# Performance work log

Hardware: AMD Instinct MI355X
Metric: run time of the kernel (lower is better)

The kernel has to match this reference:

```python
import jax, jax.numpy as jnp
import numpy as np

D_MODEL = 512
D_STATE = 64
HEADDIM = 64
EXPAND = 2
D_CONV = 4
D_INNER = EXPAND * D_MODEL            # 1024
NHEADS = D_INNER // HEADDIM           # 16
CONV_DIM = D_INNER + 2 * D_STATE      # 1152 (x, B, C share the depthwise conv)
D_IN_PROJ = 2 * D_INNER + 2 * D_STATE + NHEADS  # z, xBC, dt
C_IN = 512


def setup_inputs() -> dict:
    key = jax.random.key(0)
    ks = jax.random.split(key, 10)
    hs = jax.random.normal(ks[0], (1, C_IN, 16, 16, 16), jnp.float32)
    return {
        "hidden_states": hs,
        # 1x1 conv projections (weight stored as (out,in))
        "proj_in_w": jax.random.normal(ks[1], (D_MODEL, C_IN), jnp.float32) / np.float32(np.sqrt(C_IN)),
        "proj_in_b": jnp.zeros((D_MODEL,), jnp.float32),
        "proj_out_w": jax.random.normal(ks[2], (C_IN, D_MODEL), jnp.float32) * jnp.float32(0.02),
        "proj_out_b": jnp.zeros((C_IN,), jnp.float32),
        # Mamba2 core params
        "in_proj_w": jax.random.normal(ks[3], (D_IN_PROJ, D_MODEL), jnp.float32) / np.float32(np.sqrt(D_MODEL)),
        "conv_w": jax.random.normal(ks[4], (CONV_DIM, D_CONV), jnp.float32) / np.float32(np.sqrt(D_CONV)),
        "conv_b": jnp.zeros((CONV_DIM,), jnp.float32),
        "dt_bias": jnp.log(jnp.expm1(jax.random.uniform(ks[5], (NHEADS,), jnp.float32, 1e-3, 0.1))),
        "A_log": jnp.log(jax.random.uniform(ks[6], (NHEADS,), jnp.float32, 1.0, 16.0)),
        "D": jnp.ones((NHEADS,), jnp.float32),
        "norm_w": jnp.ones((D_INNER,), jnp.float32),
        "out_proj_w": jax.random.normal(ks[7], (D_MODEL, D_INNER), jnp.float32) / np.float32(np.sqrt(D_INNER)),
    }


def _mamba2(x, in_proj_w, conv_w, conv_b, dt_bias, A_log, Dp, norm_w, out_proj_w):
    # x: (N, T, d_model) with N = B*H*W (independent pixel sequences over time)
    N, T, _ = x.shape
    zxbcdt = jnp.einsum('ntd,ed->nte', x, in_proj_w)  # (N,T,D_IN_PROJ)
    z = zxbcdt[..., :D_INNER]
    xBC = zxbcdt[..., D_INNER:D_INNER + CONV_DIM]
    dt = zxbcdt[..., D_INNER + CONV_DIM:]             # (N,T,NHEADS)
    # causal depthwise conv along T (kernel D_CONV, left-padded), then SiLU
    pad = jnp.pad(xBC, ((0, 0), (D_CONV - 1, 0), (0, 0)))
    xc = sum(pad[:, k:k + T, :] * conv_w[:, k] for k in range(D_CONV))
    xBC = jax.nn.silu(xc + conv_b)
    xs = xBC[..., :D_INNER].reshape(N, T, NHEADS, HEADDIM)
    Bm = xBC[..., D_INNER:D_INNER + D_STATE]          # (N,T,D_STATE), ngroups=1
    Cm = xBC[..., D_INNER + D_STATE:]                 # (N,T,D_STATE)
    dt = jax.nn.softplus(dt + dt_bias)                # (N,T,NHEADS)
    A = -jnp.exp(A_log)                               # (NHEADS,)

    def step(h, inp):
        # h: (N, NHEADS, HEADDIM, D_STATE)
        dt_t, x_t, B_t, C_t = inp
        dA = jnp.exp(dt_t * A)                        # (N,NHEADS)
        h = h * dA[:, :, None, None] + (dt_t[:, :, None] * x_t)[..., None] * B_t[:, None, None, :]
        y_t = jnp.einsum('nhps,ns->nhp', h, C_t)      # (N,NHEADS,HEADDIM)
        return h, y_t

    h0 = jnp.zeros((N, NHEADS, HEADDIM, D_STATE), x.dtype)
    _, ys = jax.lax.scan(step, h0, (dt.swapaxes(0, 1), xs.swapaxes(0, 1), Bm.swapaxes(0, 1), Cm.swapaxes(0, 1)))
    y = ys.swapaxes(0, 1) + Dp[None, None, :, None] * xs   # skip term
    # gated RMSNorm: norm(y * silu(z)) * weight
    y = y.reshape(N, T, D_INNER) * jax.nn.silu(z)
    y = y * jax.lax.rsqrt(jnp.mean(y * y, axis=-1, keepdims=True) + 1e-5) * norm_w
    return jnp.einsum('ntd,od->nto', y, out_proj_w)


def reference(hidden_states, proj_in_w, proj_in_b, proj_out_w, proj_out_b,
              in_proj_w, conv_w, conv_b, dt_bias, A_log, D, norm_w, out_proj_w):
    B, C, T, H, W = hidden_states.shape
    # proj_in: 1x1 conv over channels == per-pixel matmul
    x = jnp.einsum('bcthw,dc->bthwd', hidden_states, proj_in_w) + proj_in_b
    # (B,T,H,W,D) -> (B*H*W, T, D): each pixel becomes a temporal sequence
    x = x.transpose(0, 2, 3, 1, 4).reshape(B * H * W, T, D_MODEL)
    y = _mamba2(x, in_proj_w, conv_w, conv_b, dt_bias, A_log, D, norm_w, out_proj_w)
    y = y.reshape(B, H, W, T, D_MODEL).transpose(0, 3, 1, 2, 4)  # (B,T,H,W,D)
    out = jnp.einsum('bthwd,cd->bcthw', y, proj_out_w) + proj_out_b[None, :, None, None, None]
    return (out,)
```

## Files before the change

kernel.cpp:

```cpp
#include <hip/hip_runtime.h>
#include <hip/hip_bf16.h>
#include <math.h>

#define TT       16
#define NSEQ     256
#define TOK      4096
#define DMODEL   512
#define DINNER   1024
#define DSTATE   64
#define NHEADS   16
#define HEADDIM  64
#define CONVDIM  1152
#define DINPROJ  2192
#define DTOFF    2176
#define ZLD      2176
#define NPAD_IP  2304

using bf16x8 = __attribute__((ext_vector_type(8))) short;
using f32x4  = __attribute__((ext_vector_type(4))) float;
typedef __hip_bfloat16 bf16;

__device__ __forceinline__ void gload_lds16(const void* g, void* l) {
    __builtin_amdgcn_global_load_lds(
        (const __attribute__((address_space(1))) unsigned int*)g,
        (__attribute__((address_space(3))) unsigned int*)l,
        16, 0, 0);
}

template<int NFRAG, bool OUTBF, bool DUAL, int BIAS, bool PARTSCALE>
__global__ __launch_bounds__(256) void mfma_gemm(
    const bf16* __restrict__ A, const bf16* __restrict__ B,
    const float* __restrict__ bias, const float* __restrict__ rs,
    float* __restrict__ Cf, bf16* __restrict__ Ch, float* __restrict__ C2,
    int Nreal, int K, int lda, int ldb, int ldc)
{
    constexpr int BN = NFRAG * 32;
    __shared__ short As[128 * 32];
    __shared__ short Bs[BN * 32];

    const int tid = threadIdx.x;
    const int wv = tid >> 6, ln = tid & 63;
    const int m0 = blockIdx.x * 128, n0 = blockIdx.y * BN;
    const int wr = wv >> 1, wc = wv & 1;
    const int lr = ln & 15, lk = (ln >> 4) * 8;

    f32x4 acc[4][NFRAG];
#pragma unroll
    for (int m = 0; m < 4; ++m)
#pragma unroll
        for (int n = 0; n < NFRAG; ++n) acc[m][n] = (f32x4){0.f, 0.f, 0.f, 0.f};

    for (int k0 = 0; k0 < K; k0 += 32) {
        __syncthreads();
#pragma unroll
        for (int r = 0; r < 2; ++r) {
            const int ofs = r * 4096 + tid * 16;
            const int row = ofs >> 6;
            const int ke  = (ofs & 63) >> 1;
            gload_lds16(A + (size_t)(m0 + row) * lda + k0 + ke, (char*)As + ofs);
        }
#pragma unroll
        for (int r = 0; r < NFRAG / 2; ++r) {
            const int ofs = r * 4096 + tid * 16;
            const int row = ofs >> 6;
            const int ke  = (ofs & 63) >> 1;
            gload_lds16(B + (size_t)(n0 + row) * ldb + k0 + ke, (char*)Bs + ofs);
        }
        __syncthreads();

        bf16x8 af[4], bfr[NFRAG];
#pragma unroll
        for (int m = 0; m < 4; ++m)
            af[m] = *(const bf16x8*)&As[(wr * 64 + m * 16 + lr) * 32 + lk];
#pragma unroll
        for (int n = 0; n < NFRAG; ++n)
            bfr[n] = *(const bf16x8*)&Bs[(wc * (BN / 2) + n * 16 + lr) * 32 + lk];
#pragma unroll
        for (int m = 0; m < 4; ++m)
#pragma unroll
            for (int n = 0; n < NFRAG; ++n)
                acc[m][n] = __builtin_amdgcn_mfma_f32_16x16x32_bf16(
                    af[m], bfr[n], acc[m][n], 0, 0, 0);
    }

    const int mBase = m0 + wr * 64, nBase = n0 + wc * (BN / 2);
#pragma unroll
    for (int m = 0; m < 4; ++m) {
#pragma unroll
        for (int j = 0; j < 4; ++j) {
            const int row = mBase + m * 16 + (ln >> 4) * 4 + j;
            float sc = 1.f, rb = 0.f;
            if (PARTSCALE) {
                const float4 pv = *(const float4*)(rs + (size_t)row * 4);
                sc = rsqrtf((pv.x + pv.y + pv.z + pv.w) * (1.f / 1024.f) + 1e-5f);
            }
            if (BIAS == 2) rb = bias[row];
#pragma unroll
            for (int n = 0; n < NFRAG; ++n) {
                const int col = nBase + n * 16 + lr;
                if (col < Nreal) {
                    float v = acc[m][n][j];
                    if (BIAS == 1) v += bias[col];
                    v += rb;
                    if (PARTSCALE) v *= sc;
                    if (OUTBF) {
                        Ch[(size_t)row * ldc + col] = __float2bfloat16(v);
                        if (DUAL) C2[(size_t)row * ldc + col] = v;
                    } else {
                        Cf[(size_t)row * ldc + col] = v;
                    }
                }
            }
        }
    }
}

#define SZ_PI  (512 * 512)
#define SZ_PO  (512 * 512)
#define SZ_OP  (512 * 1024)
#define SZ_IP  (DINPROJ * 512)
#define SZ_IPP (NPAD_IP * 512)
#define SZ_ALL (SZ_PI + SZ_PO + SZ_OP + SZ_IPP)
#define NB_WB  1024
#define NB_HT  2048

__global__ __launch_bounds__(256) void prep_all(
    const float* __restrict__ pi, const float* __restrict__ po,
    const float* __restrict__ op, const float* __restrict__ ip,
    const float* __restrict__ nw, const float* __restrict__ hs,
    bf16* __restrict__ wpi, bf16* __restrict__ wpo,
    bf16* __restrict__ wop, bf16* __restrict__ wip, bf16* __restrict__ hsT)
{
    __shared__ float smem[32 * 33];
    const int b = blockIdx.x, tid = threadIdx.x;

    if (b < NB_WB) {
        for (int idx = b * 256 + tid; idx < SZ_ALL; idx += NB_WB * 256) {
            if (idx < SZ_PI) {
                wpi[idx] = __float2bfloat16(pi[idx]);
            } else if (idx < SZ_PI + SZ_PO) {
                int j = idx - SZ_PI; wpo[j] = __float2bfloat16(po[j]);
            } else if (idx < SZ_PI + SZ_PO + SZ_OP) {
                int j = idx - SZ_PI - SZ_PO;
                wop[j] = __float2bfloat16(op[j] * nw[j & 1023]);
            } else {
                int j = idx - SZ_PI - SZ_PO - SZ_OP;
                wip[j] = (j < SZ_IP) ? __float2bfloat16(ip[j])
                                     : __float2bfloat16(0.f);
            }
        }
    } else {
        const int tb = b - NB_WB;
        const int v0 = (tb & 127) * 32, c0 = (tb >> 7) * 32;
        const int tx = tid & 31, ty = tid >> 5;
#pragma unroll
        for (int i = 0; i < 4; ++i)
            smem[(ty + 8 * i) * 33 + tx] =
                hs[(size_t)(c0 + ty + 8 * i) * TOK + v0 + tx];
        __syncthreads();
#pragma unroll
        for (int i = 0; i < 4; ++i)
            hsT[(size_t)(v0 + ty + 8 * i) * DMODEL + c0 + tx] =
                __float2bfloat16(smem[tx * 33 + ty + 8 * i]);
    }
}

__global__ __launch_bounds__(256) void dt_fix_kernel(
    const float* __restrict__ xv32, const float* __restrict__ in_proj_w,
    float* __restrict__ dtf)
{
    const int v = blockIdx.x;
    const int w = threadIdx.x >> 6, l = threadIdx.x & 63;
    const float4* xr = (const float4*)(xv32 + (size_t)v * DMODEL);
    const float4 x0 = xr[l * 2], x1 = xr[l * 2 + 1];
#pragma unroll
    for (int hh = 0; hh < 4; ++hh) {
        const int h = w * 4 + hh;
        const float4* wr = (const float4*)(in_proj_w + (size_t)(DTOFF + h) * DMODEL);
        const float4 w0 = wr[l * 2], w1 = wr[l * 2 + 1];
        float dot = x0.x * w0.x + x0.y * w0.y + x0.z * w0.z + x0.w * w0.w
                  + x1.x * w1.x + x1.y * w1.y + x1.z * w1.z + x1.w * w1.w;
#pragma unroll
        for (int off = 32; off >= 1; off >>= 1) dot += __shfl_xor(dot, off);
        if (l == 0) dtf[(size_t)v * 16 + h] = dot;
    }
}

__global__ __launch_bounds__(256) void ssd_kernel(
    const bf16* __restrict__ zb, const float* __restrict__ dtf,
    const float* __restrict__ conv_w, const float* __restrict__ conv_b,
    const float* __restrict__ dt_bias, const float* __restrict__ A_log,
    const float* __restrict__ Dp,
    bf16* __restrict__ gb, float* __restrict__ part)
{
    const int n = blockIdx.x, hq = blockIdx.y;
    const int tid = threadIdx.x;
    const int w = tid >> 6, p = tid & 63;
    const int h = hq * 4 + w;
    const int ch = hq * 256 + tid;

    __shared__ float Bsh[16][68];
    __shared__ float Csh[16][68];
    __shared__ float Gsh[16][16];
    __shared__ float Msh[4][256];
    __shared__ float red4[16][4];

    float ld[16];
#pragma unroll
    for (int t = 0; t < 16; ++t)
        ld[t] = __bfloat162float(zb[(size_t)(t * 256 + n) * ZLD + 1024 + ch]);

    const float cw0 = conv_w[ch * 4 + 0], cw1 = conv_w[ch * 4 + 1],
                cw2 = conv_w[ch * 4 + 2], cw3 = conv_w[ch * 4 + 3];
    const float cb = conv_b[ch];
    float xs[16];
#pragma unroll
    for (int t = 0; t < 16; ++t) {
        float a = fmaf(ld[t], cw3, cb);
        if (t >= 1) a = fmaf(ld[t - 1], cw2, a);
        if (t >= 2) a = fmaf(ld[t - 2], cw1, a);
        if (t >= 3) a = fmaf(ld[t - 3], cw0, a);
        xs[t] = a / (1.f + __expf(-a));
    }

    if (tid < 128) {
        const int cc = 1024 + tid;
        const float dw0 = conv_w[cc * 4 + 0], dw1 = conv_w[cc * 4 + 1],
                    dw2 = conv_w[cc * 4 + 2], dw3 = conv_w[cc * 4 + 3];
        const float db = conv_b[cc];
        float q0 = 0.f, q1 = 0.f, q2 = 0.f;
#pragma unroll
        for (int t = 0; t < 16; ++t) {
            const float cur =
                __bfloat162float(zb[(size_t)(t * 256 + n) * ZLD + 2048 + tid]);
            float a = fmaf(cur, dw3, db);
            a = fmaf(q2, dw2, a);
            a = fmaf(q1, dw1, a);
            a = fmaf(q0, dw0, a);
            const float val = a / (1.f + __expf(-a));
            if (tid < 64) Bsh[t][tid] = val; else Csh[t][tid - 64] = val;
            q0 = q1; q1 = q2; q2 = cur;
        }
    }

    const float a_h = -__expf(A_log[h]);
    float dtv_l = 0.f;
    if (p < 16) {
        const float raw = dtf[(size_t)(p * 256 + n) * 16 + h] + dt_bias[h];
        dtv_l = (raw > 20.f) ? raw : log1pf(__expf(raw));
    }
    float cum_l = dtv_l;
#pragma unroll
    for (int off = 1; off < 16; off <<= 1) {
        const float tmp = __shfl_up(cum_l, off);
        if (p >= off) cum_l += tmp;
    }
    __syncthreads();

    {
        const int t = tid >> 4, s = tid & 15;
        float acc = 0.f;
#pragma unroll
        for (int k = 0; k < 64; ++k)
            acc = fmaf(Csh[t][k], Bsh[s][k], acc);
        Gsh[t][s] = acc;
    }
    __syncthreads();

    float dtv_all[16], cum_all[16];
#pragma unroll
    for (int t = 0; t < 16; ++t) {
        dtv_all[t] = __shfl(dtv_l, t);
        cum_all[t] = __shfl(cum_l, t);
    }
#pragma unroll
    for (int q = 0; q < 4; ++q) {
        const int idx = p * 4 + q;
        const int t = idx >> 4, s = idx & 15;
        float m = 0.f;
        if (s <= t)
            m = __expf(a_h * (cum_all[t] - cum_all[s])) * Gsh[t][s] * dtv_all[s];
        Msh[w][idx] = m;
    }

    float zl[16];
#pragma unroll
    for (int t = 0; t < 16; ++t)
        zl[t] = __bfloat162float(zb[(size_t)(t * 256 + n) * ZLD + ch]);

    const float Dh = Dp[h];
    float g[16];
#pragma unroll
    for (int t = 0; t < 16; ++t) {
        float y = 0.f;
#pragma unroll
        for (int s = 0; s <= t; ++s)
            y = fmaf(Msh[w][t * 16 + s], xs[s], y);
        y = fmaf(Dh, xs[t], y);
        g[t] = y * (zl[t] / (1.f + __expf(-zl[t])));
    }

#pragma unroll
    for (int t = 0; t < 16; ++t) {
        float ss = g[t] * g[t];
#pragma unroll
        for (int off = 32; off >= 1; off >>= 1) ss += __shfl_xor(ss, off);
        if (p == 0) red4[t][w] = ss;
        gb[(size_t)(t * 256 + n) * DINNER + ch] = __float2bfloat16(g[t]);
    }
    __syncthreads();
    if (tid < 16)
        part[(size_t)(tid * 256 + n) * 4 + hq] =
            red4[tid][0] + red4[tid][1] + red4[tid][2] + red4[tid][3];
}

extern "C" void kernel_launch(void* const* d_in, const int* in_sizes, int n_in,
                              void* d_out, int out_size, void* d_ws, size_t ws_size,
                              hipStream_t stream) {
    const float* hs         = (const float*)d_in[0];
    const float* proj_in_w  = (const float*)d_in[1];
    const float* proj_in_b  = (const float*)d_in[2];
    const float* proj_out_w = (const float*)d_in[3];
    const float* proj_out_b = (const float*)d_in[4];
    const float* in_proj_w  = (const float*)d_in[5];
    const float* conv_w     = (const float*)d_in[6];
    const float* conv_b     = (const float*)d_in[7];
    const float* dt_bias    = (const float*)d_in[8];
    const float* A_log      = (const float*)d_in[9];
    const float* Dp         = (const float*)d_in[10];
    const float* norm_w     = (const float*)d_in[11];
    const float* out_proj_w = (const float*)d_in[12];
    float* out = (float*)d_out;

    float* ws      = (float*)d_ws;
    float* dtf     = ws;
    float* part    = dtf + (size_t)TOK * 16;
    float* xv32    = part + (size_t)TOK * 4;
    bf16*  hsT     = (bf16*)(xv32 + (size_t)TOK * DMODEL);
    bf16*  xv_bf   = hsT + (size_t)TOK * DMODEL;
    bf16*  zb      = xv_bf + (size_t)TOK * DMODEL;
    bf16*  gb      = zb + (size_t)TOK * ZLD;
    bf16*  y2      = gb + (size_t)TOK * DINNER;
    bf16*  wpi     = y2 + (size_t)TOK * DMODEL;
    bf16*  wpo     = wpi + SZ_PI;
    bf16*  wop     = wpo + SZ_PO;
    bf16*  wip     = wop + SZ_OP;

    prep_all<<<NB_WB + NB_HT, 256, 0, stream>>>(
        proj_in_w, proj_out_w, out_proj_w, in_proj_w, norm_w, hs,
        wpi, wpo, wop, wip, hsT);

    mfma_gemm<2, true, true, 1, false><<<dim3(32, 8), 256, 0, stream>>>(
        hsT, wpi, proj_in_b, nullptr, nullptr, xv_bf, xv32,
        DMODEL, DMODEL, DMODEL, DMODEL, DMODEL);

    mfma_gemm<4, true, false, 0, false><<<dim3(32, 18), 256, 0, stream>>>(
        xv_bf, wip, nullptr, nullptr, nullptr, zb, nullptr,
        ZLD, DMODEL, DMODEL, DMODEL, ZLD);

    dt_fix_kernel<<<TOK, 256, 0, stream>>>(xv32, in_proj_w, dtf);

    ssd_kernel<<<dim3(NSEQ, 4), 256, 0, stream>>>(
        zb, dtf, conv_w, conv_b, dt_bias, A_log, Dp, gb, part);

    mfma_gemm<2, true, false, 0, true><<<dim3(32, 8), 256, 0, stream>>>(
        gb, wop, nullptr, part, nullptr, y2, nullptr,
        DMODEL, DINNER, DINNER, DINNER, DMODEL);

    mfma_gemm<2, false, false, 2, false><<<dim3(4, 64), 256, 0, stream>>>(
        wpo, y2, proj_out_b, nullptr, out, nullptr, nullptr,
        TOK, DMODEL, DMODEL, DMODEL, TOK);
}
```

Measured before the change: 121.2 us.

## Fold out_proj into proj_out weights to fuse the last two GEMMs

Precomputes a combined weight Wbig = proj_out_w · (out_proj_w·diag(norm_w)) with a small extra GEMM, then runs a single GEMM of K=1024 from the gated activations straight to the output. The per-token RMSNorm scale moves into the epilogue as a column scale. This removes the intermediate y2 write and read plus one launch, but adds a weight-product GEMM on every call and changes rounding, since the product is stored in bf16. It also hoists the column bias and scale loads out of the epilogue loop.

```diff
diff --git a/kernel.cpp b/kernel.cpp
--- a/kernel.cpp
+++ b/kernel.cpp
@@ -27,7 +27,7 @@
         16, 0, 0);
 }
 
-template<int NFRAG, bool OUTBF, bool DUAL, int BIAS, bool PARTSCALE>
+template<int NFRAG, bool OUTBF, bool DUAL, int BIAS, bool PARTSCALE, bool COLSCALE>
 __global__ __launch_bounds__(256) void mfma_gemm(
     const bf16* __restrict__ A, const bf16* __restrict__ B,
     const float* __restrict__ bias, const float* __restrict__ rs,
@@ -84,6 +84,21 @@
     }
 
     const int mBase = m0 + wr * 64, nBase = n0 + wc * (BN / 2);
+
+    float scn[NFRAG], cbv[NFRAG];
+#pragma unroll
+    for (int n = 0; n < NFRAG; ++n) {
+        const int col = nBase + n * 16 + lr;
+        scn[n] = 1.f; cbv[n] = 0.f;
+        if (col < Nreal) {
+            if (COLSCALE) {
+                const float4 pv = *(const float4*)(rs + (size_t)col * 4);
+                scn[n] = rsqrtf((pv.x + pv.y + pv.z + pv.w) * (1.f / 1024.f) + 1e-5f);
+            }
+            if (BIAS == 1) cbv[n] = bias[col];
+        }
+    }
+
 #pragma unroll
     for (int m = 0; m < 4; ++m) {
 #pragma unroll
@@ -100,9 +115,9 @@
                 const int col = nBase + n * 16 + lr;
                 if (col < Nreal) {
                     float v = acc[m][n][j];
-                    if (BIAS == 1) v += bias[col];
-                    v += rb;
                     if (PARTSCALE) v *= sc;
+                    if (COLSCALE)  v *= scn[n];
+                    v += cbv[n] + rb;
                     if (OUTBF) {
                         Ch[(size_t)row * ldc + col] = __float2bfloat16(v);
                         if (DUAL) C2[(size_t)row * ldc + col] = v;
@@ -117,19 +132,19 @@
 
 #define SZ_PI  (512 * 512)
 #define SZ_PO  (512 * 512)
-#define SZ_OP  (512 * 1024)
 #define SZ_IP  (DINPROJ * 512)
 #define SZ_IPP (NPAD_IP * 512)
-#define SZ_ALL (SZ_PI + SZ_PO + SZ_OP + SZ_IPP)
-#define NB_WB  1024
+#define SZ_ALL (SZ_PI + SZ_PO + SZ_IPP)
+#define NB_WB  768
+#define NB_WT  512
 #define NB_HT  2048
 
 __global__ __launch_bounds__(256) void prep_all(
     const float* __restrict__ pi, const float* __restrict__ po,
     const float* __restrict__ op, const float* __restrict__ ip,
     const float* __restrict__ nw, const float* __restrict__ hs,
-    bf16* __restrict__ wpi, bf16* __restrict__ wpo,
-    bf16* __restrict__ wop, bf16* __restrict__ wip, bf16* __restrict__ hsT)
+    bf16* __restrict__ wpi, bf16* __restrict__ wpo, bf16* __restrict__ wip,
+    bf16* __restrict__ wopT, bf16* __restrict__ hsT)
 {
     __shared__ float smem[32 * 33];
     const int b = blockIdx.x, tid = threadIdx.x;
@@ -140,17 +155,29 @@
                 wpi[idx] = __float2bfloat16(pi[idx]);
             } else if (idx < SZ_PI + SZ_PO) {
                 int j = idx - SZ_PI; wpo[j] = __float2bfloat16(po[j]);
-            } else if (idx < SZ_PI + SZ_PO + SZ_OP) {
+            } else {
                 int j = idx - SZ_PI - SZ_PO;
-                wop[j] = __float2bfloat16(op[j] * nw[j & 1023]);
-            } else {
-                int j = idx - SZ_PI - SZ_PO - SZ_OP;
                 wip[j] = (j < SZ_IP) ? __float2bfloat16(ip[j])
                                      : __float2bfloat16(0.f);
             }
         }
+    } else if (b < NB_WB + NB_WT) {
+        const int tb = b - NB_WB;
+        const int o0 = (tb & 15) * 32, d0 = (tb >> 4) * 32;
+        const int tx = tid & 31, ty = tid >> 5;
+#pragma unroll
+        for (int i = 0; i < 4; ++i)
+            smem[(ty + 8 * i) * 33 + tx] =
+                op[(size_t)(o0 + ty + 8 * i) * DINNER + d0 + tx];
+        __syncthreads();
+#pragma unroll
+        for (int i = 0; i < 4; ++i) {
+            const int d = d0 + ty + 8 * i;
+            wopT[(size_t)d * DMODEL + o0 + tx] =
+                __float2bfloat16(smem[tx * 33 + ty + 8 * i] * nw[d]);
+        }
     } else {
-        const int tb = b - NB_WB;
+        const int tb = b - NB_WB - NB_WT;
         const int v0 = (tb & 127) * 32, c0 = (tb >> 7) * 32;
         const int tx = tid & 31, ty = tid >> 5;
 #pragma unroll
@@ -340,21 +367,25 @@
     bf16*  xv_bf   = hsT + (size_t)TOK * DMODEL;
     bf16*  zb      = xv_bf + (size_t)TOK * DMODEL;
     bf16*  gb      = zb + (size_t)TOK * ZLD;
-    bf16*  y2      = gb + (size_t)TOK * DINNER;
-    bf16*  wpi     = y2 + (size_t)TOK * DMODEL;
+    bf16*  wpi     = gb + (size_t)TOK * DINNER;
     bf16*  wpo     = wpi + SZ_PI;
-    bf16*  wop     = wpo + SZ_PO;
-    bf16*  wip     = wop + SZ_OP;
-
-    prep_all<<<NB_WB + NB_HT, 256, 0, stream>>>(
+    bf16*  wip     = wpo + SZ_PO;
+    bf16*  wopT    = wip + SZ_IPP;
+    bf16*  Wbig    = wopT + (size_t)DINNER * DMODEL;
+
+    prep_all<<<NB_WB + NB_WT + NB_HT, 256, 0, stream>>>(
         proj_in_w, proj_out_w, out_proj_w, in_proj_w, norm_w, hs,
-        wpi, wpo, wop, wip, hsT);
-
-    mfma_gemm<2, true, true, 1, false><<<dim3(32, 8), 256, 0, stream>>>(
+        wpi, wpo, wip, wopT, hsT);
+
+    mfma_gemm<2, true, false, 0, false, false><<<dim3(4, 16), 256, 0, stream>>>(
+        wpo, wopT, nullptr, nullptr, nullptr, Wbig, nullptr,
+        DINNER, DMODEL, DMODEL, DMODEL, DINNER);
+
+    mfma_gemm<2, true, true, 1, false, false><<<dim3(32, 8), 256, 0, stream>>>(
         hsT, wpi, proj_in_b, nullptr, nullptr, xv_bf, xv32,
         DMODEL, DMODEL, DMODEL, DMODEL, DMODEL);
 
-    mfma_gemm<4, true, false, 0, false><<<dim3(32, 18), 256, 0, stream>>>(
+    mfma_gemm<4, true, false, 0, false, false><<<dim3(32, 18), 256, 0, stream>>>(
         xv_bf, wip, nullptr, nullptr, nullptr, zb, nullptr,
         ZLD, DMODEL, DMODEL, DMODEL, ZLD);
 
@@ -363,11 +394,7 @@
     ssd_kernel<<<dim3(NSEQ, 4), 256, 0, stream>>>(
         zb, dtf, conv_w, conv_b, dt_bias, A_log, Dp, gb, part);
 
-    mfma_gemm<2, true, false, 0, true><<<dim3(32, 8), 256, 0, stream>>>(
-        gb, wop, nullptr, part, nullptr, y2, nullptr,
-        DMODEL, DINNER, DINNER, DINNER, DMODEL);
-
-    mfma_gemm<2, false, false, 2, false><<<dim3(4, 64), 256, 0, stream>>>(
-        wpo, y2, proj_out_b, nullptr, out, nullptr, nullptr,
-        TOK, DMODEL, DMODEL, DMODEL, TOK);
-}
+    mfma_gemm<2, false, false, 2, false, true><<<dim3(4, 64), 256, 0, stream>>>(
+        Wbig, gb, proj_out_b, part, out, nullptr, nullptr,
+        TOK, DINNER, DINNER, DINNER, TOK);
+}
```

Measured after the change: 117.8 us, median of 2. 2.8% less time.
